# Optimization experiments

Measured on AMD Instinct MI355X. Metric: run time of the kernel, lower is better.

## Reference

```python
import jax, jax.numpy as jnp
from jax import lax
import numpy as np

KSIZE = 3        # patch-matching kernel
RATE = 2         # dilation/upsample rate
FUSE_K = 3       # fusion kernel size
SCALE = 10.0     # softmax scale
EPS = 1e-4


def _same_pads(size, k, s):
    # TF 'SAME' padding: total pad so out = ceil(size / s)
    out = -(-size // s)
    total = max(0, (out - 1) * s + k - size)
    top = total // 2
    return (top, total - top)


def _extract_patches(x, k, s):
    # x: [N,C,H,W] -> [N, L, C, k, k], SAME padding, row-major patch order
    ph = _same_pads(x.shape[2], k, s)
    pw = _same_pads(x.shape[3], k, s)
    p = lax.conv_general_dilated_patches(x, (k, k), (s, s), (ph, pw))
    N, _, Ho, Wo = p.shape
    C = x.shape[1]
    p = p.reshape(N, C, k, k, Ho * Wo)  # channel-major patch layout (matches torch unfold)
    return jnp.transpose(p, (0, 4, 1, 2, 3))


def setup_inputs() -> dict:
    key = jax.random.key(0)
    k1, k2 = jax.random.split(key)
    f = jax.random.normal(k1, (8, 96, 64, 64), dtype=jnp.float32)
    b = jax.random.normal(k2, (8, 96, 64, 64), dtype=jnp.float32)
    return {"f": f, "b": b}


def reference(f, b):
    # TF-style nearest-neighbor downsample (stride sampling)
    fs = f[:, :, ::RATE, ::RATE]
    bs = b[:, :, ::RATE, ::RATE]
    N, C, H, W = fs.shape  # downsampled dims; f and b share shape here
    L = H * W
    kernel = 2 * RATE

    # raw background patches for aggregation: [N, L, C, 2r, 2r]
    raw_w = _extract_patches(b, kernel, RATE)
    # matching patches from downsampled background: [N, L, C, 3, 3]
    w = _extract_patches(bs, KSIZE, 1)

    fuse_w = jnp.eye(FUSE_K, dtype=f.dtype).reshape(1, 1, FUSE_K, FUSE_K)
    ct_pad = kernel - 1 - 1  # conv_transpose padding=1 -> conv pad k-1-p = 2

    def attend(xi, wi, rwi):
        # xi: [C,H,W]; wi: [L,C,3,3]; rwi: [L,C,2r,2r]
        norm = jnp.sqrt(jnp.sum(wi * wi, axis=(1, 2, 3), keepdims=True))
        wn = wi / jnp.maximum(norm, EPS)
        # cosine-similarity correlation: [L,H,W]
        yi = lax.conv_general_dilated(xi[None], wn, (1, 1), ((1, 1), (1, 1)))[0]
        # fusion: identity-kernel convs over the [L_b, L_f] score map, both orientations
        y2 = yi.reshape(1, 1, L, L)
        y2 = lax.conv_general_dilated(y2, fuse_w, (1, 1), ((1, 1), (1, 1)))
        y2 = jnp.transpose(y2.reshape(H, W, H, W), (1, 0, 3, 2)).reshape(1, 1, L, L)
        y2 = lax.conv_general_dilated(y2, fuse_w, (1, 1), ((1, 1), (1, 1)))
        yi = jnp.transpose(y2.reshape(W, H, W, H), (1, 0, 3, 2)).reshape(L, H, W)
        # softmax over background patches (mask mm == 1 since mask is None)
        yi = jax.nn.softmax(yi * SCALE, axis=0)
        # conv_transpose2d(yi, rwi, stride=RATE, padding=1) / 4
        wct = jnp.flip(jnp.swapaxes(rwi, 0, 1), axis=(2, 3))  # [C, L, 2r, 2r]
        out = lax.conv_general_dilated(
            yi[None], wct, (1, 1), ((ct_pad, ct_pad), (ct_pad, ct_pad)),
            lhs_dilation=(RATE, RATE))[0]
        return out / 4.0

    y = jax.vmap(attend)(fs, w, raw_w)  # [N, C, H*RATE, W*RATE]
    return y.reshape(f.shape)
```

## Files before the change

kernel.cpp:

```cpp
#include <hip/hip_runtime.h>
#include <math.h>

#define NB 8
#define NC 96
#define HF 64
#define HS 32
#define L 1024
#define MN 1536

#define G_OFF    0ull
#define F1T_OFF  (8ull * 1024 * 1024)
#define YB_B     (64ull * 1024 * 1024)
#define RWT_B    (80ull * 1024 * 1024)
#define N_OFF    (27262976ull)
#define FS_OFF   (27271168ull)
#define BS_OFF   (28057600ull)
#define Z_OFF    0ull

typedef __attribute__((ext_vector_type(8))) short short8;
typedef __attribute__((ext_vector_type(4))) float float4v;

__device__ inline unsigned short f2bf(float x) {
    union { float f; unsigned u; } v; v.f = x;
    unsigned r = v.u + 0x7fff + ((v.u >> 16) & 1);
    return (unsigned short)(r >> 16);
}

__global__ void kpre_pack(const float* __restrict__ f, const float* __restrict__ b,
                          float* __restrict__ ws) {
    int n = blockIdx.x, c = blockIdx.y, which = blockIdx.z;
    const float* src = (which ? b : f) + ((size_t)n * NC + c) * (HF * HF);
    float* dst = ws + (which ? BS_OFF : FS_OFF) + ((size_t)n * NC + c) * 1024;
    int t = threadIdx.x;
    #pragma unroll
    for (int e = 0; e < 4; ++e) {
        int pos = t + e * 256;
        int i = pos >> 5, j = pos & 31;
        dst[pos] = src[(2 * i) * HF + 2 * j];
    }
}

__global__ void k0_norm(float* __restrict__ ws) {
    int n = blockIdx.x;
    int t = threadIdx.x;
    int i = t >> 5, j = t & 31;
    __shared__ float sq[1024];
    const float* bsp = ws + BS_OFF + (size_t)n * NC * 1024;
    float s = 0.f;
    for (int c = 0; c < NC; ++c) {
        float v = bsp[(size_t)c * 1024 + t];
        s += v * v;
    }
    sq[t] = s;
    __syncthreads();
    float nsq = 0.f;
    #pragma unroll
    for (int dy = -1; dy <= 1; ++dy)
        #pragma unroll
        for (int dx = -1; dx <= 1; ++dx) {
            int ii = i + dy, jj = j + dx;
            if (ii >= 0 && ii < HS && jj >= 0 && jj < HS) nsq += sq[ii * HS + jj];
        }
    ws[N_OFF + (size_t)n * L + t] = 1.f / fmaxf(sqrtf(nsq), 1e-4f);
}

__global__ __launch_bounds__(256) void k1_gram(float* __restrict__ ws) {
    int n = blockIdx.x;
    int p0 = blockIdx.y * 128, l0 = blockIdx.z * 128;
    int t = threadIdx.x;
    int tp = t >> 4, tm = t & 15;
    __shared__ float Bt[32][132];
    __shared__ float Ft[32][132];
    float acc[8][8] = {};
    const float* bsp = ws + BS_OFF + (size_t)n * NC * 1024;
    const float* fsp = ws + FS_OFF + (size_t)n * NC * 1024;
    for (int c0 = 0; c0 < NC; c0 += 32) {
        #pragma unroll
        for (int e = 0; e < 4; ++e) {
            int idx = t + e * 256;
            int cl = idx >> 5, vq = idx & 31;
            *(float4*)&Bt[cl][vq * 4] =
                *(const float4*)&bsp[(size_t)(c0 + cl) * 1024 + l0 + vq * 4];
            *(float4*)&Ft[cl][vq * 4] =
                *(const float4*)&fsp[(size_t)(c0 + cl) * 1024 + p0 + vq * 4];
        }
        __syncthreads();
        for (int cl = 0; cl < 32; ++cl) {
            float4 a0 = *(const float4*)&Bt[cl][tp * 8];
            float4 a1 = *(const float4*)&Bt[cl][tp * 8 + 4];
            float4 b0 = *(const float4*)&Ft[cl][tm * 8];
            float4 b1 = *(const float4*)&Ft[cl][tm * 8 + 4];
            float av[8] = {a0.x, a0.y, a0.z, a0.w, a1.x, a1.y, a1.z, a1.w};
            float bv[8] = {b0.x, b0.y, b0.z, b0.w, b1.x, b1.y, b1.z, b1.w};
            #pragma unroll
            for (int aa = 0; aa < 8; ++aa)
                #pragma unroll
                for (int bb = 0; bb < 8; ++bb)
                    acc[aa][bb] += av[aa] * bv[bb];
        }
        __syncthreads();
    }
    float* G = ws + G_OFF + (size_t)n * L * L;
    #pragma unroll
    for (int aa = 0; aa < 8; ++aa) {
        int l = l0 + tp * 8 + aa;
        *(float4*)&G[(size_t)l * L + p0 + tm * 8] =
            make_float4(acc[aa][0], acc[aa][1], acc[aa][2], acc[aa][3]);
        *(float4*)&G[(size_t)l * L + p0 + tm * 8 + 4] =
            make_float4(acc[aa][4], acc[aa][5], acc[aa][6], acc[aa][7]);
    }
}

__global__ __launch_bounds__(256) void k23_score_fuse1t(float* __restrict__ ws) {
    int bid = blockIdx.x;
    int n = bid & 7;
    int tile = bid >> 3;
    int i0 = (tile >> 5) * 32, j0 = (tile & 31) * 32;
    int t = threadIdx.x;
    __shared__ float U[36][37];
    __shared__ float sA[34][35];
    __shared__ float sinv[34];
    const float* G = ws + G_OFF + (size_t)n * L * L;
    const float* invn = ws + N_OFF + (size_t)n * L;
    if (t < 34) {
        int l = i0 - 1 + t;
        sinv[t] = ((unsigned)l < L) ? invn[l] : 0.f;
    }
    for (int e = 0; e < 6; ++e) {
        int idx = t + e * 256;
        if (idx < 1296) {
            int a = idx / 36, bq = idx - a * 36;
            int l = i0 - 2 + a, p = j0 - 2 + bq;
            float s = 0.f;
            #pragma unroll
            for (int dy = -1; dy <= 1; ++dy) {
                int ll = l + dy * 32, pp = p + dy * 32;
                if ((unsigned)ll < L && (unsigned)pp < L)
                    s += G[(size_t)ll * L + pp];
            }
            U[a][bq] = s;
        }
    }
    __syncthreads();
    for (int e = 0; e < 5; ++e) {
        int idx = t + e * 256;
        if (idx < 1156) {
            int ih = idx / 34, jh = idx - ih * 34;
            int l = i0 - 1 + ih, p = j0 - 1 + jh;
            float a = 0.f;
            if ((unsigned)l < L && (unsigned)p < L) {
                int lx = l & 31, px = p & 31;
                float s = 0.f;
                #pragma unroll
                for (int dx = -1; dx <= 1; ++dx) {
                    bool ok = (unsigned)(lx + dx) < HS && (unsigned)(px + dx) < HS;
                    float u = U[ih + 1 + dx][jh + 1 + dx];
                    s += ok ? u : 0.f;
                }
                a = sinv[ih] * s;
            }
            sA[ih][jh] = a;
        }
    }
    __syncthreads();
    float* F1T = ws + F1T_OFF + (size_t)n * L * L;
    #pragma unroll
    for (int e = 0; e < 4; ++e) {
        int idx = t + e * 256;
        int jl = idx >> 5, il = idx & 31;
        float v = sA[il][jl] + sA[il + 1][jl + 1] + sA[il + 2][jl + 2];
        F1T[(size_t)(j0 + jl) * L + i0 + il] = v;
    }
}

__global__ void k4_fuse2_softmax(float* __restrict__ ws) {
    int bid = blockIdx.x;
    int n = bid & 7, p = bid >> 3;
    int t = threadIdx.x;
    int py = p >> 5, px = p & 31;
    int Jc = px * HS + py;
    __shared__ float s3[3][32][33];
    __shared__ float red[8];
    const float* F1T = ws + F1T_OFF + (size_t)n * L * L;
    #pragma unroll
    for (int d = 0; d < 3; ++d) {
        int Jd = Jc + d - 1;
        bool ok = (Jd >= 0 && Jd < L);
        int rd = ok ? ((Jd & 31) * HS + (Jd >> 5)) : 0;
        const float* row = F1T + (size_t)rd * L;
        for (int e = 0; e < 4; ++e) {
            int i_ = t + e * 256;
            float v = ok ? row[i_] : 0.f;
            s3[d][i_ & 31][i_ >> 5] = v;
        }
    }
    __syncthreads();
    float vals[4];
    float mymax = -1e30f;
    #pragma unroll
    for (int e = 0; e < 4; ++e) {
        int kk = t + e * 256;
        float v = 0.f;
        #pragma unroll
        for (int d = 0; d < 3; ++d) {
            int kd = kk + d - 1;
            if (kd >= 0 && kd < L) v += s3[d][kd >> 5][kd & 31];
        }
        v *= 10.0f;
        vals[e] = v;
        mymax = fmaxf(mymax, v);
    }
    #pragma unroll
    for (int off = 32; off > 0; off >>= 1)
        mymax = fmaxf(mymax, __shfl_xor(mymax, off));
    if ((t & 63) == 0) red[t >> 6] = mymax;
    __syncthreads();
    float Mx = fmaxf(fmaxf(red[0], red[1]), fmaxf(red[2], red[3]));
    float mysum = 0.f;
    #pragma unroll
    for (int e = 0; e < 4; ++e) { vals[e] = __expf(vals[e] - Mx); mysum += vals[e]; }
    #pragma unroll
    for (int off = 32; off > 0; off >>= 1)
        mysum += __shfl_xor(mysum, off);
    if ((t & 63) == 0) red[4 + (t >> 6)] = mysum;
    __syncthreads();
    float rinv = 1.f / (red[4] + red[5] + red[6] + red[7]);
    unsigned short* Yb = (unsigned short*)((char*)ws + YB_B) + (size_t)n * L * L + (size_t)p * L;
    #pragma unroll
    for (int e = 0; e < 4; ++e) Yb[t + e * 256] = f2bf(vals[e] * rinv);
}

__global__ void k5_rwt(const float* __restrict__ b, float* __restrict__ ws) {
    int n = blockIdx.x, c = blockIdx.y;
    int t = threadIdx.x;
    __shared__ float pl[64][65];
    const float* bp = b + ((size_t)n * NC + c) * (HF * HF);
    for (int e = 0; e < 16; ++e) {
        int idx = t + e * 256;
        pl[idx >> 6][idx & 63] = bp[idx];
    }
    __syncthreads();
    unsigned short* RWt = (unsigned short*)((char*)ws + RWT_B) + ((size_t)n * MN + c * 16) * L;
    #pragma unroll
    for (int uv = 0; uv < 16; ++uv) {
        int u = uv >> 2, v = uv & 3;
        for (int e = 0; e < 4; ++e) {
            int k = t + e * 256;
            int ly = k & 31, lx = k >> 5;
            int r = 2 * ly - 1 + u, s = 2 * lx - 1 + v;
            float val = (r >= 0 && r < HF && s >= 0 && s < HF) ? pl[r][s] : 0.f;
            RWt[(size_t)uv * L + k] = f2bf(val);
        }
    }
}

__global__ __launch_bounds__(256) void k6_mfma_z(float* __restrict__ ws) {
    int n = blockIdx.x;
    int m0 = blockIdx.y * 128;
    int p0 = blockIdx.z * 128;
    int t = threadIdx.x;
    int lane = t & 63, wv = t >> 6;
    int wp = (wv >> 1) * 64, wm = (wv & 1) * 64;
    int fr = lane & 15, qd = lane >> 4;

    __shared__ unsigned short As[128][72];
    __shared__ unsigned short Bs[128][72];

    const unsigned short* Ybp = (const unsigned short*)((const char*)ws + YB_B) + (size_t)n * L * L;
    const unsigned short* RWtp = (const unsigned short*)((const char*)ws + RWT_B) + (size_t)n * MN * L;

    float4v acc[4][4] = {};

    for (int k0 = 0; k0 < L; k0 += 64) {
        __syncthreads();
        #pragma unroll
        for (int e = 0; e < 4; ++e) {
            int id = t + e * 256;
            int row = id >> 3, cb = id & 7;
            *(short8*)&As[row][cb * 8] =
                *(const short8*)(Ybp + (size_t)(p0 + row) * L + k0 + cb * 8);
            *(short8*)&Bs[row][cb * 8] =
                *(const short8*)(RWtp + (size_t)(m0 + row) * L + k0 + cb * 8);
        }
        __syncthreads();
        #pragma unroll
        for (int ks = 0; ks < 2; ++ks) {
            short8 af[4], bf[4];
            #pragma unroll
            for (int a = 0; a < 4; ++a)
                af[a] = *(const short8*)&As[wp + a * 16 + fr][ks * 32 + qd * 8];
            #pragma unroll
            for (int bq = 0; bq < 4; ++bq)
                bf[bq] = *(const short8*)&Bs[wm + bq * 16 + fr][ks * 32 + qd * 8];
            #pragma unroll
            for (int a = 0; a < 4; ++a)
                #pragma unroll
                for (int bq = 0; bq < 4; ++bq)
                    acc[a][bq] = __builtin_amdgcn_mfma_f32_16x16x32_bf16(
                        af[a], bf[bq], acc[a][bq], 0, 0, 0);
        }
    }

    float* Zp = ws + Z_OFF + (size_t)n * L * MN;
    #pragma unroll
    for (int a = 0; a < 4; ++a) {
        #pragma unroll
        for (int r = 0; r < 4; ++r) {
            int p = p0 + wp + a * 16 + qd * 4 + r;
            #pragma unroll
            for (int bq = 0; bq < 4; ++bq) {
                int m = m0 + wm + bq * 16 + fr;
                Zp[(size_t)p * MN + m] = acc[a][bq][r];
            }
        }
    }
}

__global__ __launch_bounds__(256) void k7_gather(const float* __restrict__ ws,
                                                 float* __restrict__ out) {
    int n = blockIdx.x, yq = blockIdx.y, c = blockIdx.z;
    int t = threadIdx.x;
    int y0 = yq * 4;
    int ibase = (y0 >> 1) - 1;
    __shared__ float zs[128][17];
    const float* Zp = ws + Z_OFF + (size_t)n * L * MN;
    #pragma unroll
    for (int e = 0; e < 2; ++e) {
        int idx = t + e * 256;
        int pl = idx >> 2, q = idx & 3;
        int il = pl >> 5, j = pl & 31;
        int i = ibase + il;
        float4 v = make_float4(0.f, 0.f, 0.f, 0.f);
        if (i >= 0 && i < HS)
            v = *(const float4*)&Zp[(size_t)(i * HS + j) * MN + c * 16 + q * 4];
        zs[pl][q * 4 + 0] = v.x;
        zs[pl][q * 4 + 1] = v.y;
        zs[pl][q * 4 + 2] = v.z;
        zs[pl][q * 4 + 3] = v.w;
    }
    __syncthreads();
    int y = y0 + (t >> 6), x = t & 63;
    int ih = (y + 1) >> 1, jh = (x + 1) >> 1;
    float s = 0.f;
    #pragma unroll
    for (int di = 0; di < 2; ++di) {
        int i = ih - di;
        if (i < 0 || i >= HS) continue;
        int u = y + 1 - 2 * i;
        int il = i - ibase;
        #pragma unroll
        for (int dj = 0; dj < 2; ++dj) {
            int j = jh - dj;
            if (j < 0 || j >= HS) continue;
            int v = x + 1 - 2 * j;
            s += zs[il * 32 + j][u * 4 + v];
        }
    }
    out[(((size_t)n * NC + c) * HF + y) * HF + x] = 0.25f * s;
}

extern "C" void kernel_launch(void* const* d_in, const int* in_sizes, int n_in,
                              void* d_out, int out_size, void* d_ws, size_t ws_size,
                              hipStream_t stream) {
    const float* f = (const float*)d_in[0];
    const float* b = (const float*)d_in[1];
    float* out = (float*)d_out;
    float* ws = (float*)d_ws;

    kpre_pack<<<dim3(NB, NC, 2), 256, 0, stream>>>(f, b, ws);
    k0_norm<<<NB, 1024, 0, stream>>>(ws);
    k1_gram<<<dim3(NB, 8, 8), 256, 0, stream>>>(ws);
    k23_score_fuse1t<<<8192, 256, 0, stream>>>(ws);
    k4_fuse2_softmax<<<8192, 256, 0, stream>>>(ws);
    k5_rwt<<<dim3(NB, NC), 256, 0, stream>>>(b, ws);
    k6_mfma_z<<<dim3(NB, 12, 8), 256, 0, stream>>>(ws);
    k7_gather<<<dim3(NB, 16, NC), 256, 0, stream>>>(ws, out);
}
```

Before: 217.9 us.

## Pre-swizzle GEMM operands into MFMA fragment layout and drop LDS staging

The softmax and raw-weight kernels now write their bf16 outputs directly in the per-lane MFMA fragment order (16-row tiles by 32-wide k-chunks). The GEMM kernel then loads each wave's fragments straight from global memory with coalesced 16-byte loads and register double-buffering, removing shared-memory staging and block-level barriers. The trade-off is no intra-block operand sharing through LDS, so each wave loads its own A/B tiles and relies on L2 for reuse, plus scattered stores in the producer kernels.

After: 209.6 us. 3.8% less time.

```diff
diff --git a/kernel.cpp b/kernel.cpp
--- a/kernel.cpp
+++ b/kernel.cpp
@@ -225,9 +225,14 @@
     if ((t & 63) == 0) red[4 + (t >> 6)] = mysum;
     __syncthreads();
     float rinv = 1.f / (red[4] + red[5] + red[6] + red[7]);
-    unsigned short* Yb = (unsigned short*)((char*)ws + YB_B) + (size_t)n * L * L + (size_t)p * L;
-    #pragma unroll
-    for (int e = 0; e < 4; ++e) Yb[t + e * 256] = f2bf(vals[e] * rinv);
+    unsigned short* YbF = (unsigned short*)((char*)ws + YB_B) + (size_t)n * L * L;
+    int pt = p >> 4, fr = p & 15;
+    #pragma unroll
+    for (int e = 0; e < 4; ++e) {
+        int kk = t + e * 256;
+        int kc = kk >> 5, qd = (kk >> 3) & 3, j = kk & 7;
+        YbF[((size_t)pt * 32 + kc) * 512 + (qd * 16 + fr) * 8 + j] = f2bf(vals[e] * rinv);
+    }
 }
 
 __global__ void k5_rwt(const float* __restrict__ b, float* __restrict__ ws) {
@@ -240,7 +245,8 @@
         pl[idx >> 6][idx & 63] = bp[idx];
     }
     __syncthreads();
-    unsigned short* RWt = (unsigned short*)((char*)ws + RWT_B) + ((size_t)n * MN + c * 16) * L;
+    unsigned short* RWtF = (unsigned short*)((char*)ws + RWT_B) + (size_t)n * MN * L
+                           + (size_t)c * 32 * 512;
     #pragma unroll
     for (int uv = 0; uv < 16; ++uv) {
         int u = uv >> 2, v = uv & 3;
@@ -249,67 +255,57 @@
             int ly = k & 31, lx = k >> 5;
             int r = 2 * ly - 1 + u, s = 2 * lx - 1 + v;
             float val = (r >= 0 && r < HF && s >= 0 && s < HF) ? pl[r][s] : 0.f;
-            RWt[(size_t)uv * L + k] = f2bf(val);
+            int kc = k >> 5, qd = (k >> 3) & 3, j = k & 7;
+            RWtF[(size_t)kc * 512 + (qd * 16 + uv) * 8 + j] = f2bf(val);
         }
     }
 }
 
 __global__ __launch_bounds__(256) void k6_mfma_z(float* __restrict__ ws) {
     int n = blockIdx.x;
-    int m0 = blockIdx.y * 128;
-    int p0 = blockIdx.z * 128;
-    int t = threadIdx.x;
-    int lane = t & 63, wv = t >> 6;
-    int wp = (wv >> 1) * 64, wm = (wv & 1) * 64;
+    int wv = threadIdx.x >> 6, lane = threadIdx.x & 63;
+    int pt0 = blockIdx.z * 8 + (wv >> 1) * 4;
+    int mt0 = blockIdx.y * 8 + (wv & 1) * 4;
+
+    const unsigned short* YbF = (const unsigned short*)((const char*)ws + YB_B)
+                                + (size_t)n * L * L + lane * 8;
+    const unsigned short* RWtF = (const unsigned short*)((const char*)ws + RWT_B)
+                                 + (size_t)n * MN * L + lane * 8;
+
+    float4v acc[4][4] = {};
+    short8 af[2][4], bf[2][4];
+    #pragma unroll
+    for (int a = 0; a < 4; ++a) {
+        af[0][a] = *(const short8*)(YbF + ((size_t)(pt0 + a) * 32) * 512);
+        bf[0][a] = *(const short8*)(RWtF + ((size_t)(mt0 + a) * 32) * 512);
+    }
+    for (int kc = 0; kc < 32; ++kc) {
+        int cur = kc & 1, nxt = cur ^ 1;
+        if (kc < 31) {
+            #pragma unroll
+            for (int a = 0; a < 4; ++a) {
+                af[nxt][a] = *(const short8*)(YbF + ((size_t)(pt0 + a) * 32 + kc + 1) * 512);
+                bf[nxt][a] = *(const short8*)(RWtF + ((size_t)(mt0 + a) * 32 + kc + 1) * 512);
+            }
+        }
+        #pragma unroll
+        for (int a = 0; a < 4; ++a)
+            #pragma unroll
+            for (int bq = 0; bq < 4; ++bq)
+                acc[a][bq] = __builtin_amdgcn_mfma_f32_16x16x32_bf16(
+                    af[cur][a], bf[cur][bq], acc[a][bq], 0, 0, 0);
+    }
+
     int fr = lane & 15, qd = lane >> 4;
-
-    __shared__ unsigned short As[128][72];
-    __shared__ unsigned short Bs[128][72];
-
-    const unsigned short* Ybp = (const unsigned short*)((const char*)ws + YB_B) + (size_t)n * L * L;
-    const unsigned short* RWtp = (const unsigned short*)((const char*)ws + RWT_B) + (size_t)n * MN * L;
-
-    float4v acc[4][4] = {};
-
-    for (int k0 = 0; k0 < L; k0 += 64) {
-        __syncthreads();
-        #pragma unroll
-        for (int e = 0; e < 4; ++e) {
-            int id = t + e * 256;
-            int row = id >> 3, cb = id & 7;
-            *(short8*)&As[row][cb * 8] =
-                *(const short8*)(Ybp + (size_t)(p0 + row) * L + k0 + cb * 8);
-            *(short8*)&Bs[row][cb * 8] =
-                *(const short8*)(RWtp + (size_t)(m0 + row) * L + k0 + cb * 8);
-        }
-        __syncthreads();
-        #pragma unroll
-        for (int ks = 0; ks < 2; ++ks) {
-            short8 af[4], bf[4];
-            #pragma unroll
-            for (int a = 0; a < 4; ++a)
-                af[a] = *(const short8*)&As[wp + a * 16 + fr][ks * 32 + qd * 8];
-            #pragma unroll
-            for (int bq = 0; bq < 4; ++bq)
-                bf[bq] = *(const short8*)&Bs[wm + bq * 16 + fr][ks * 32 + qd * 8];
-            #pragma unroll
-            for (int a = 0; a < 4; ++a)
-                #pragma unroll
-                for (int bq = 0; bq < 4; ++bq)
-                    acc[a][bq] = __builtin_amdgcn_mfma_f32_16x16x32_bf16(
-                        af[a], bf[bq], acc[a][bq], 0, 0, 0);
-        }
-    }
-
     float* Zp = ws + Z_OFF + (size_t)n * L * MN;
     #pragma unroll
     for (int a = 0; a < 4; ++a) {
         #pragma unroll
         for (int r = 0; r < 4; ++r) {
-            int p = p0 + wp + a * 16 + qd * 4 + r;
+            int p = (pt0 + a) * 16 + qd * 4 + r;
             #pragma unroll
             for (int bq = 0; bq < 4; ++bq) {
-                int m = m0 + wm + bq * 16 + fr;
+                int m = (mt0 + bq) * 16 + fr;
                 Zp[(size_t)p * MN + m] = acc[a][bq][r];
             }
         }
```
